# Performance work log

Hardware: AMD Instinct MI355X
Metric: run time of the kernel (lower is better)

Reference implementation:

```python
import jax, jax.numpy as jnp
import numpy as np

NUM_TRAIN = 256  # num_train_anchors
N, A, T = 8, 131072, 64


def _make_boxes(key, shape2):
    # shape2 = (..., 2) of (y, x); returns valid boxes (y1, x1, y2, x2) in [0, 1]
    k1, k2 = jax.random.split(key)
    c1 = jax.random.uniform(k1, shape2, dtype=jnp.float32)
    c2 = jax.random.uniform(k2, shape2, dtype=jnp.float32)
    lo = jnp.minimum(c1, c2)
    hi = jnp.maximum(c1, c2)
    return jnp.stack([lo[..., 0], lo[..., 1], hi[..., 0], hi[..., 1]], axis=-1)


def setup_inputs() -> dict:
    key = jax.random.key(0)
    ka, kt, kp, kn = jax.random.split(key, 4)
    return {
        "anchors": _make_boxes(ka, (N, A, 2)),
        "true_bboxes": _make_boxes(kt, (N, T, 2)),
        "rand_pos": jax.random.uniform(kp, (N, A), dtype=jnp.float32),
        "rand_neg": jax.random.uniform(kn, (N, A), dtype=jnp.float32),
    }


def _bbox_overlap(anchors, gt):
    # anchors [A,4], gt [T,4] -> IoU [A,T]
    ay1, ax1, ay2, ax2 = [anchors[:, i] for i in range(4)]
    gy1, gx1, gy2, gx2 = [gt[:, i] for i in range(4)]
    a_area = (ay2 - ay1) * (ax2 - ax1)                       # [A]
    g_area = (gy2 - gy1) * (gx2 - gx1)                       # [T]
    ih = jnp.clip(jnp.minimum(ay2[:, None], gy2[None, :]) - jnp.maximum(ay1[:, None], gy1[None, :]), 0.0)
    iw = jnp.clip(jnp.minimum(ax2[:, None], gx2[None, :]) - jnp.maximum(ax1[:, None], gx1[None, :]), 0.0)
    inter = ih * iw                                          # [A,T]
    union = a_area[:, None] + g_area[None, :] - inter
    return jnp.where(union > 0, inter / jnp.where(union > 0, union, 1.0), 0.0)


def _rank_of(scores):
    # rank[i] = position of element i in ascending sort of scores
    order = jnp.argsort(scores)
    return jnp.zeros(scores.shape[0], jnp.int32).at[order].set(jnp.arange(scores.shape[0], dtype=jnp.int32))


def _compute_bbox_deltas(anchors, gt):
    # standard (dy, dx, dh, dw) encoding with safe denominators
    ah = anchors[:, 2] - anchors[:, 0]
    aw = anchors[:, 3] - anchors[:, 1]
    acy = anchors[:, 0] + 0.5 * ah
    acx = anchors[:, 1] + 0.5 * aw
    gh = gt[:, 2] - gt[:, 0]
    gw = gt[:, 3] - gt[:, 1]
    gcy = gt[:, 0] + 0.5 * gh
    gcx = gt[:, 1] + 0.5 * gw
    ah_s = jnp.where(ah > 0, ah, 1.0)
    aw_s = jnp.where(aw > 0, aw, 1.0)
    gh_s = jnp.where(gh > 0, gh, 1.0)
    gw_s = jnp.where(gw > 0, gw, 1.0)
    return jnp.stack([(gcy - acy) / ah_s, (gcx - acx) / aw_s,
                      jnp.log(gh_s / ah_s), jnp.log(gw_s / aw_s)], axis=-1)


def _get_targets(anchors, gt, r_pos, r_neg):
    na = anchors.shape[0]
    # strip_out_of_bounds_anchors: zero out anchors falling outside [0,1]^2 (keeps static shape)
    inb = (anchors[:, 0] >= 0) & (anchors[:, 1] >= 0) & (anchors[:, 2] <= 1) & (anchors[:, 3] <= 1)
    anchors = jnp.where(inb[:, None], anchors, 0.0)

    overlaps = _bbox_overlap(anchors, gt)                    # [A,T]

    # --- class assignment ---
    iou_max_val = jnp.max(overlaps, axis=1)                  # [A]
    classes = jnp.full((na,), -1, jnp.int32)
    classes = jnp.where(iou_max_val < 0.3, 0, classes)
    iou_max_anchor = jnp.argmax(overlaps, axis=0)            # [T] best anchor per gt
    pos_anchor = jnp.zeros((na,), jnp.int32).at[iou_max_anchor].set(1)
    classes = jnp.where(pos_anchor > 0, 1, classes)
    classes = jnp.where(iou_max_val >= 0.7, 1, classes)

    # --- subsample positives to NUM_TRAIN//2 (uniform random subset) ---
    pos = classes > 0
    rank_p = _rank_of(jnp.where(pos, r_pos, jnp.inf))
    keep_pos = pos & (rank_p < NUM_TRAIN // 2)
    classes = jnp.where(pos & ~keep_pos, -1, classes)
    n_pos = jnp.sum(keep_pos.astype(jnp.int32))

    # --- subsample negatives to NUM_TRAIN - n_pos ---
    desired_neg = NUM_TRAIN - n_pos
    neg = classes == 0
    rank_n = _rank_of(jnp.where(neg, r_neg, jnp.inf))
    keep_neg = neg & (rank_n < desired_neg)
    classes = jnp.where(neg & ~keep_neg, -1, classes)

    # --- deltas for positive anchors ---
    best_gt = jnp.argmax(overlaps, axis=1)                   # [A]
    deltas = _compute_bbox_deltas(anchors, gt[best_gt])      # [A,4]
    deltas = jnp.where((classes > 0)[:, None], deltas, 0.0)
    return classes, deltas


def reference(anchors, true_bboxes, rand_pos, rand_neg):
    classes, deltas = jax.vmap(_get_targets)(anchors, true_bboxes, rand_pos, rand_neg)
    return classes, deltas
```

## Files before the change

kernel.cpp:

```cpp
#include <hip/hip_runtime.h>
#include <stdint.h>

#define N_B 8
#define A_N 131072
#define T_N 64
#define NUM_TRAIN 256
#define POS_CAP 65536
#define NEG_CAP 32768
#define NEG_TAU 0.05f
#define NB2 256
#define ITEM_CAP 1024
#define APT 4
#define GBLK (A_N / (256 * APT))
#define BLK_C (A_N / (256 * 4))

typedef unsigned long long u64;
typedef unsigned int u32;

__device__ __forceinline__ float iou_one(float ay1, float ax1, float ay2, float ax2,
                                         float a_area, float gy1, float gx1, float gy2,
                                         float gx2, float g_area) {
#pragma clang fp contract(off)
    float ih = fmaxf(fminf(ay2, gy2) - fmaxf(ay1, gy1), 0.0f);
    float iw = fmaxf(fminf(ax2, gx2) - fmaxf(ax1, gx1), 0.0f);
    float inter = ih * iw;
    float uni = (a_area + g_area) - inter;
    return uni > 0.0f ? inter / uni : 0.0f;
}

__global__ void __launch_bounds__(256, 4) k_main(const float4* __restrict__ anchors4,
                                                 const float4* __restrict__ gts4,
                                                 unsigned char* __restrict__ preclass,
                                                 u64* __restrict__ colpart) {
    __shared__ float4 gbox[T_N];
    __shared__ float gars[T_N];
    __shared__ u64 cmax[T_N];
    int n = blockIdx.y, tid = threadIdx.x, lane = tid & 63;
    int a0 = blockIdx.x * (256 * APT) + tid;
    if (tid < T_N) {
        float4 gb = gts4[n * T_N + tid];
        gbox[tid] = gb;
        {
#pragma clang fp contract(off)
            gars[tid] = (gb.z - gb.x) * (gb.w - gb.y);
        }
        cmax[tid] = 0xFFFFFFFFull;
    }
    __syncthreads();

    float ay1[APT], ax1[APT], ay2[APT], ax2[APT], aar[APT], vmax[APT];
#pragma unroll
    for (int k = 0; k < APT; k++) {
        float4 ab = anchors4[(size_t)n * A_N + a0 + k * 256];
        float y1 = ab.x, x1 = ab.y, y2 = ab.z, x2 = ab.w;
        bool inb = (y1 >= 0.f) && (x1 >= 0.f) && (y2 <= 1.f) && (x2 <= 1.f);
        if (!inb) { y1 = x1 = y2 = x2 = 0.f; }
        ay1[k] = y1; ax1[k] = x1; ay2[k] = y2; ax2[k] = x2;
        {
#pragma clang fp contract(off)
            aar[k] = (y2 - y1) * (x2 - x1);
        }
        vmax[k] = 0.f;
    }

#pragma unroll 2
    for (int jj = 0; jj < T_N; jj++) {
        int j = (lane + jj) & (T_N - 1);
        float4 gb = gbox[j];
        float gar = gars[j];
        u64 colc = 0;
#pragma unroll
        for (int k = 0; k < APT; k++) {
            float v = iou_one(ay1[k], ax1[k], ay2[k], ax2[k], aar[k],
                              gb.x, gb.y, gb.z, gb.w, gar);
            vmax[k] = fmaxf(vmax[k], v);
            u64 pcv = ((u64)__float_as_uint(v) << 32) | (u32)(~(u32)(a0 + k * 256));
            colc = pcv > colc ? pcv : colc;
        }
        atomicMax(&cmax[j], colc);
    }

#pragma unroll
    for (int k = 0; k < APT; k++) {
        float vm = vmax[k];
        int c0 = (vm < 0.3f) ? 0 : ((vm >= 0.7f) ? 1 : -1);
        preclass[(size_t)n * A_N + a0 + k * 256] = (unsigned char)(signed char)c0;
    }
    __syncthreads();
    if (tid < T_N) colpart[((size_t)n * T_N + tid) * GBLK + blockIdx.x] = cmax[tid];
}

__global__ void k_colred(const u64* __restrict__ colpart, int* __restrict__ wnr) {
    int w = blockIdx.x * 4 + (threadIdx.x >> 6);
    int lane = threadIdx.x & 63;
    const u64* p = colpart + (size_t)w * GBLK;
    u64 m = p[lane];
    u64 m2 = p[lane + 64];
    m = m2 > m ? m2 : m;
#pragma unroll
    for (int off = 32; off > 0; off >>= 1) {
        u64 o = (u64)__shfl_xor((unsigned long long)m, off, 64);
        m = o > m ? o : m;
    }
    if (lane == 0) wnr[w] = (int)(~(u32)(m & 0xFFFFFFFFull));
}

__global__ void __launch_bounds__(256) k_classify(const u32* __restrict__ preclass32,
                                                  const int* __restrict__ wnr,
                                                  const float4* __restrict__ rneg4,
                                                  u32* __restrict__ class32,
                                                  int* __restrict__ bcp, int* __restrict__ bcn) {
    __shared__ int wnrs[T_N];
    __shared__ int wp[4], wn[4];
    int n = blockIdx.y, bx = blockIdx.x, tid = threadIdx.x;
    if (tid < T_N) wnrs[tid] = wnr[n * T_N + tid];
    __syncthreads();

    size_t gi4 = ((size_t)n * A_N) / 4 + bx * 256 + tid;
    u32 pcw = preclass32[gi4];
    float4 rn = rneg4[gi4];
    int a0 = (bx * 256 + tid) * 4;

    u32 marked = 0;
#pragma unroll
    for (int t = 0; t < T_N; t++) {
        u32 d = (u32)(wnrs[t] - a0);
        if (d < 4u) marked |= 1u << d;
    }

    float rnv[4] = {rn.x, rn.y, rn.z, rn.w};
    int pcnt = 0, ncnt = 0;
    u32 cw = 0;
#pragma unroll
    for (int j = 0; j < 4; j++) {
        int c = (int)(signed char)((pcw >> (8 * j)) & 0xFF);
        if ((marked >> j) & 1) c = 1;
        cw |= ((u32)(unsigned char)(signed char)c) << (8 * j);
        pcnt += (c == 1);
        ncnt += (c == 0 && rnv[j] < NEG_TAU);
    }
    class32[gi4] = cw;

#pragma unroll
    for (int off = 32; off > 0; off >>= 1) {
        pcnt += __shfl_xor(pcnt, off, 64);
        ncnt += __shfl_xor(ncnt, off, 64);
    }
    if ((tid & 63) == 0) { wp[tid >> 6] = pcnt; wn[tid >> 6] = ncnt; }
    __syncthreads();
    if (tid == 0) {
        bcp[n * BLK_C + bx] = wp[0] + wp[1] + wp[2] + wp[3];
        bcn[n * BLK_C + bx] = wn[0] + wn[1] + wn[2] + wn[3];
    }
}

__global__ void __launch_bounds__(256) k_gather(const u32* __restrict__ class32,
                                                const float4* __restrict__ rpos4,
                                                const float4* __restrict__ rneg4,
                                                const int* __restrict__ bcp,
                                                const int* __restrict__ bcn,
                                                u64* __restrict__ pos_list,
                                                u64* __restrict__ neg_list) {
    __shared__ int sp[BLK_C], sn[BLK_C];
    __shared__ int lp, ln;
    int n = blockIdx.y, bx = blockIdx.x, tid = threadIdx.x;
    if (tid == 0) { lp = 0; ln = 0; }
    if (tid < BLK_C) { sp[tid] = bcp[n * BLK_C + tid]; sn[tid] = bcn[n * BLK_C + tid]; }
    __syncthreads();
    for (int d = 1; d < BLK_C; d <<= 1) {
        int vp = 0, vn = 0;
        if (tid < BLK_C && tid >= d) { vp = sp[tid - d]; vn = sn[tid - d]; }
        __syncthreads();
        if (tid < BLK_C) { sp[tid] += vp; sn[tid] += vn; }
        __syncthreads();
    }
    int bp = bx ? sp[bx - 1] : 0;
    int bn = bx ? sn[bx - 1] : 0;

    size_t gi4 = ((size_t)n * A_N) / 4 + bx * 256 + tid;
    u32 cw = class32[gi4];
    float4 rp = rpos4[gi4];
    float4 rn = rneg4[gi4];
    float rpv[4] = {rp.x, rp.y, rp.z, rp.w};
    float rnv[4] = {rn.x, rn.y, rn.z, rn.w};
    int a0 = (bx * 256 + tid) * 4;

#pragma unroll
    for (int j = 0; j < 4; j++) {
        int c = (int)(signed char)((cw >> (8 * j)) & 0xFF);
        int a = a0 + j;
        if (c == 1) {
            int slot = atomicAdd(&lp, 1);
            int i = bp + slot;
            if (i < POS_CAP)
                pos_list[n * POS_CAP + i] = ((u64)__float_as_uint(rpv[j]) << 32) | (u32)a;
        } else if (c == 0 && rnv[j] < NEG_TAU) {
            int slot = atomicAdd(&ln, 1);
            int i = bn + slot;
            if (i < NEG_CAP)
                neg_list[n * NEG_CAP + i] = ((u64)__float_as_uint(rnv[j]) << 32) | (u32)a;
        }
    }
}

__device__ u64 select_kth(const u64* list, int cnt, int k, float scale, u64 ovf,
                          int* hist, u64* items, int* misc, u64* result, int* wsum) {
    int tid = threadIdx.x, lane = tid & 63, wid = tid >> 6;
    if (k >= cnt) return ovf;

    hist[tid] = 0;
    if (tid == 0) { misc[0] = 0; *result = ovf; }
    __syncthreads();

    for (int i = tid; i < cnt; i += 256) {
        float v = __uint_as_float((u32)(list[i] >> 32));
        int b = (int)(v * scale); b = b < NB2 - 1 ? b : NB2 - 1;
        atomicAdd(&hist[b], 1);
    }
    __syncthreads();

    int h = hist[tid];
    int v = h;
#pragma unroll
    for (int d = 1; d < 64; d <<= 1) {
        int t = __shfl_up(v, d, 64);
        if (lane >= d) v += t;
    }
    if (lane == 63) wsum[wid] = v;
    __syncthreads();
    int base = 0;
    for (int w = 0; w < wid; w++) base += wsum[w];
    int incl = base + v, excl = incl - h;
    if (k >= excl && k < incl) { misc[1] = tid; misc[2] = excl; }
    __syncthreads();
    int b = misc[1], before = misc[2];

    for (int i = tid; i < cnt; i += 256) {
        u64 p = list[i];
        float vv = __uint_as_float((u32)(p >> 32));
        int bb = (int)(vv * scale); bb = bb < NB2 - 1 ? bb : NB2 - 1;
        if (bb == b) { int ix = atomicAdd(&misc[0], 1); if (ix < ITEM_CAP) items[ix] = p; }
    }
    __syncthreads();
    int m = misc[0]; m = m < ITEM_CAP ? m : ITEM_CAP;
    int target = k - before;
    for (int i = tid; i < m; i += 256) {
        u64 p = items[i];
        int r = 0;
        for (int j = 0; j < m; j++) r += (items[j] < p);
        if (r == target) *result = p;
    }
    __syncthreads();
    u64 res = *result;
    __syncthreads();
    return res;
}

__global__ void k_select(const u64* __restrict__ pos_list, const u64* __restrict__ neg_list,
                         const int* __restrict__ bcp, const int* __restrict__ bcn,
                         u64* __restrict__ cutoff) {
    __shared__ int hist[NB2];
    __shared__ u64 items[ITEM_CAP];
    __shared__ int misc[3];
    __shared__ u64 result;
    __shared__ int wsum[4];
    __shared__ int pw[4], nw[4];
    int n = blockIdx.x, tid = threadIdx.x;

    int pv = (tid < BLK_C) ? bcp[n * BLK_C + tid] : 0;
    int nv = (tid < BLK_C) ? bcn[n * BLK_C + tid] : 0;
#pragma unroll
    for (int off = 32; off > 0; off >>= 1) {
        pv += __shfl_xor(pv, off, 64);
        nv += __shfl_xor(nv, off, 64);
    }
    if ((tid & 63) == 0) { pw[tid >> 6] = pv; nw[tid >> 6] = nv; }
    __syncthreads();
    int P = pw[0] + pw[1] + pw[2] + pw[3];
    int C = nw[0] + nw[1] + nw[2] + nw[3];
    int Pc = P < POS_CAP ? P : POS_CAP;
    int Cc = C < NEG_CAP ? C : NEG_CAP;

    u64 cpos = select_kth(pos_list + n * POS_CAP, Pc, NUM_TRAIN / 2, (float)NB2,
                          0xFFFFFFFFFFFFFFFFull, hist, items, misc, &result, wsum);
    int n_pos = P < NUM_TRAIN / 2 ? P : NUM_TRAIN / 2;
    int k_neg = NUM_TRAIN - n_pos;
    u64 cneg = select_kth(neg_list + n * NEG_CAP, Cc, k_neg, (float)NB2 / NEG_TAU,
                          ((u64)__float_as_uint(NEG_TAU) << 32), hist, items, misc, &result, wsum);
    if (tid == 0) { cutoff[2 * n] = cpos; cutoff[2 * n + 1] = cneg; }
}

__global__ void __launch_bounds__(256) k_final(const float4* __restrict__ anchors4,
                                               const float4* __restrict__ gts4,
                                               const u32* __restrict__ class32,
                                               const float4* __restrict__ rpos4,
                                               const float4* __restrict__ rneg4,
                                               const u64* __restrict__ cutoff,
                                               float4* __restrict__ out_classes4,
                                               float4* __restrict__ out_deltas) {
    __shared__ float4 gbox[T_N];
    __shared__ float gars[T_N];
    int n = blockIdx.y, bx = blockIdx.x, tid = threadIdx.x;
    if (tid < T_N) {
        float4 gb = gts4[n * T_N + tid];
        gbox[tid] = gb;
        {
#pragma clang fp contract(off)
            gars[tid] = (gb.z - gb.x) * (gb.w - gb.y);
        }
    }
    __syncthreads();

    size_t gi4 = ((size_t)n * A_N) / 4 + bx * 256 + tid;
    u32 cw = class32[gi4];
    float4 rp = rpos4[gi4];
    float4 rn = rneg4[gi4];
    float rpv[4] = {rp.x, rp.y, rp.z, rp.w};
    float rnv[4] = {rn.x, rn.y, rn.z, rn.w};
    int a0 = (bx * 256 + tid) * 4;
    u64 cp = cutoff[2 * n], cn = cutoff[2 * n + 1];

    float fcv[4];
#pragma unroll
    for (int j = 0; j < 4; j++) {
        int c = (int)(signed char)((cw >> (8 * j)) & 0xFF);
        int a = a0 + j;
        int fc = -1;
        if (c == 1) {
            u64 p = ((u64)__float_as_uint(rpv[j]) << 32) | (u32)a;
            fc = (p < cp) ? 1 : -1;
        } else if (c == 0) {
            u64 p = ((u64)__float_as_uint(rnv[j]) << 32) | (u32)a;
            fc = (p < cn) ? 0 : -1;
        }
        fcv[j] = (float)fc;

        float4 d = make_float4(0.f, 0.f, 0.f, 0.f);
        if (fc == 1) {
            float4 ab = anchors4[(size_t)n * A_N + a];
            float ay1 = ab.x, ax1 = ab.y, ay2 = ab.z, ax2 = ab.w;
            bool inb = (ay1 >= 0.f) && (ax1 >= 0.f) && (ay2 <= 1.f) && (ax2 <= 1.f);
            if (!inb) { ay1 = ax1 = ay2 = ax2 = 0.f; }
            float a_area;
            {
#pragma clang fp contract(off)
                a_area = (ay2 - ay1) * (ax2 - ax1);
            }
            float vm = 0.f; int jb = 0;
            for (int t = 0; t < T_N; t++) {
                float4 gb = gbox[t];
                float v = iou_one(ay1, ax1, ay2, ax2, a_area, gb.x, gb.y, gb.z, gb.w, gars[t]);
                bool g = v > vm;
                vm = g ? v : vm;
                jb = g ? t : jb;
            }
            float4 gb = gbox[jb];
            float gy1 = gb.x, gx1 = gb.y, gy2 = gb.z, gx2 = gb.w;
            float ah = ay2 - ay1, aw = ax2 - ax1;
            float acy = ay1 + 0.5f * ah, acx = ax1 + 0.5f * aw;
            float gh = gy2 - gy1, gw = gx2 - gx1;
            float gcy = gy1 + 0.5f * gh, gcx = gx1 + 0.5f * gw;
            float ah_s = ah > 0.f ? ah : 1.f, aw_s = aw > 0.f ? aw : 1.f;
            float gh_s = gh > 0.f ? gh : 1.f, gw_s = gw > 0.f ? gw : 1.f;
            d.x = (gcy - acy) / ah_s;
            d.y = (gcx - acx) / aw_s;
            d.z = logf(gh_s / ah_s);
            d.w = logf(gw_s / aw_s);
        }
        out_deltas[(size_t)n * A_N + a] = d;
    }
    out_classes4[gi4] = make_float4(fcv[0], fcv[1], fcv[2], fcv[3]);
}

extern "C" void kernel_launch(void* const* d_in, const int* in_sizes, int n_in,
                              void* d_out, int out_size, void* d_ws, size_t ws_size,
                              hipStream_t stream) {
    const float* anchors = (const float*)d_in[0];
    const float* gts     = (const float*)d_in[1];
    const float* rpos    = (const float*)d_in[2];
    const float* rneg    = (const float*)d_in[3];

    char* p = (char*)d_ws;
    u64* cutoff   = (u64*)p;  p += 2 * N_B * sizeof(u64);
    u64* colpart  = (u64*)p;  p += (size_t)N_B * T_N * GBLK * sizeof(u64);
    u64* pos_list = (u64*)p;  p += (size_t)N_B * POS_CAP * sizeof(u64);
    u64* neg_list = (u64*)p;  p += (size_t)N_B * NEG_CAP * sizeof(u64);
    u32* preclass = (u32*)p;  p += (size_t)N_B * A_N;
    u32* class_f  = (u32*)p;  p += (size_t)N_B * A_N;
    int* bcp  = (int*)p;  p += N_B * BLK_C * sizeof(int);
    int* bcn  = (int*)p;  p += N_B * BLK_C * sizeof(int);
    int* wnr  = (int*)p;  p += N_B * T_N * sizeof(int);

    float* out_classes = (float*)d_out;
    float4* out_deltas = (float4*)(out_classes + (size_t)N_B * A_N);

    k_main<<<dim3(GBLK, N_B), 256, 0, stream>>>(
        (const float4*)anchors, (const float4*)gts, (unsigned char*)preclass, colpart);
    k_colred<<<N_B * T_N / 4, 256, 0, stream>>>(colpart, wnr);
    k_classify<<<dim3(BLK_C, N_B), 256, 0, stream>>>(
        preclass, wnr, (const float4*)rneg, class_f, bcp, bcn);
    k_gather<<<dim3(BLK_C, N_B), 256, 0, stream>>>(
        class_f, (const float4*)rpos, (const float4*)rneg, bcp, bcn, pos_list, neg_list);
    k_select<<<N_B, 256, 0, stream>>>(pos_list, neg_list, bcp, bcn, cutoff);
    k_final<<<dim3(BLK_C, N_B), 256, 0, stream>>>(
        (const float4*)anchors, (const float4*)gts, class_f,
        (const float4*)rpos, (const float4*)rneg, cutoff,
        (float4*)out_classes, out_deltas);
}
```

Measured before the change: 187.6 us.

## Fuse candidate gathering into IoU kernel and fold column reduction into select

The IoU kernel now writes positive and negative candidates straight into per-block segmented lists and records per-block counts. This removes the separate classify and gather passes and the colred kernel. The select kernel reduces the per-column argmax itself, adds the column-winner anchors as extra positives, and excludes them from the negative lists while it builds histograms. Six launches become three, and several full passes over classes and random values disappear. In exchange, select walks 128 segments per image and does a 64-way exclusion check for each negative candidate, and the inner IoU loop tracks a per-thread column argmax with a deeper unroll.

```diff
diff --git a/kernel.cpp b/kernel.cpp
--- a/kernel.cpp
+++ b/kernel.cpp
@@ -5,14 +5,11 @@
 #define A_N 131072
 #define T_N 64
 #define NUM_TRAIN 256
-#define POS_CAP 65536
-#define NEG_CAP 32768
 #define NEG_TAU 0.05f
-#define NB2 256
 #define ITEM_CAP 1024
 #define APT 4
-#define GBLK (A_N / (256 * APT))
-#define BLK_C (A_N / (256 * 4))
+#define GBLK 128
+#define SEG 1024
 
 typedef unsigned long long u64;
 typedef unsigned int u32;
@@ -30,13 +27,21 @@
 
 __global__ void __launch_bounds__(256, 4) k_main(const float4* __restrict__ anchors4,
                                                  const float4* __restrict__ gts4,
+                                                 const float* __restrict__ rpos,
+                                                 const float* __restrict__ rneg,
                                                  unsigned char* __restrict__ preclass,
-                                                 u64* __restrict__ colpart) {
+                                                 u64* __restrict__ colpart,
+                                                 u64* __restrict__ pos_list,
+                                                 u64* __restrict__ neg_list,
+                                                 int* __restrict__ bcp, int* __restrict__ bcn) {
     __shared__ float4 gbox[T_N];
     __shared__ float gars[T_N];
     __shared__ u64 cmax[T_N];
-    int n = blockIdx.y, tid = threadIdx.x, lane = tid & 63;
-    int a0 = blockIdx.x * (256 * APT) + tid;
+    __shared__ int lp, ln;
+    int n = blockIdx.y, bx = blockIdx.x, tid = threadIdx.x, lane = tid & 63;
+    int a0 = bx * SEG + tid;
+    size_t nA = (size_t)n * A_N;
+
     if (tid < T_N) {
         float4 gb = gts4[n * T_N + tid];
         gbox[tid] = gb;
@@ -44,14 +49,15 @@
 #pragma clang fp contract(off)
             gars[tid] = (gb.z - gb.x) * (gb.w - gb.y);
         }
-        cmax[tid] = 0xFFFFFFFFull;
-    }
+        cmax[tid] = 0;
+    }
+    if (tid == 0) { lp = 0; ln = 0; }
     __syncthreads();
 
     float ay1[APT], ax1[APT], ay2[APT], ax2[APT], aar[APT], vmax[APT];
 #pragma unroll
     for (int k = 0; k < APT; k++) {
-        float4 ab = anchors4[(size_t)n * A_N + a0 + k * 256];
+        float4 ab = anchors4[nA + a0 + k * 256];
         float y1 = ab.x, x1 = ab.y, y2 = ab.z, x2 = ab.w;
         bool inb = (y1 >= 0.f) && (x1 >= 0.f) && (y2 <= 1.f) && (x2 <= 1.f);
         if (!inb) { y1 = x1 = y2 = x2 = 0.f; }
@@ -63,164 +69,80 @@
         vmax[k] = 0.f;
     }
 
-#pragma unroll 2
+#pragma unroll 4
     for (int jj = 0; jj < T_N; jj++) {
         int j = (lane + jj) & (T_N - 1);
         float4 gb = gbox[j];
         float gar = gars[j];
-        u64 colc = 0;
-#pragma unroll
-        for (int k = 0; k < APT; k++) {
-            float v = iou_one(ay1[k], ax1[k], ay2[k], ax2[k], aar[k],
-                              gb.x, gb.y, gb.z, gb.w, gar);
+        float vb = iou_one(ay1[0], ax1[0], ay2[0], ax2[0], aar[0], gb.x, gb.y, gb.z, gb.w, gar);
+        vmax[0] = fmaxf(vmax[0], vb);
+        int kb = 0;
+#pragma unroll
+        for (int k = 1; k < APT; k++) {
+            float v = iou_one(ay1[k], ax1[k], ay2[k], ax2[k], aar[k], gb.x, gb.y, gb.z, gb.w, gar);
             vmax[k] = fmaxf(vmax[k], v);
-            u64 pcv = ((u64)__float_as_uint(v) << 32) | (u32)(~(u32)(a0 + k * 256));
-            colc = pcv > colc ? pcv : colc;
-        }
-        atomicMax(&cmax[j], colc);
-    }
-
+            if (v > vb) { vb = v; kb = k; }
+        }
+        u64 pk = ((u64)__float_as_uint(vb) << 32) | (u32)(~(u32)(a0 + (kb << 8)));
+        atomicMax(&cmax[j], pk);
+    }
+
+    size_t segbase = ((size_t)(n * GBLK + bx)) << 10;
 #pragma unroll
     for (int k = 0; k < APT; k++) {
+        int a = a0 + k * 256;
         float vm = vmax[k];
         int c0 = (vm < 0.3f) ? 0 : ((vm >= 0.7f) ? 1 : -1);
-        preclass[(size_t)n * A_N + a0 + k * 256] = (unsigned char)(signed char)c0;
-    }
-    __syncthreads();
-    if (tid < T_N) colpart[((size_t)n * T_N + tid) * GBLK + blockIdx.x] = cmax[tid];
-}
-
-__global__ void k_colred(const u64* __restrict__ colpart, int* __restrict__ wnr) {
-    int w = blockIdx.x * 4 + (threadIdx.x >> 6);
-    int lane = threadIdx.x & 63;
-    const u64* p = colpart + (size_t)w * GBLK;
-    u64 m = p[lane];
-    u64 m2 = p[lane + 64];
-    m = m2 > m ? m2 : m;
-#pragma unroll
-    for (int off = 32; off > 0; off >>= 1) {
-        u64 o = (u64)__shfl_xor((unsigned long long)m, off, 64);
-        m = o > m ? o : m;
-    }
-    if (lane == 0) wnr[w] = (int)(~(u32)(m & 0xFFFFFFFFull));
-}
-
-__global__ void __launch_bounds__(256) k_classify(const u32* __restrict__ preclass32,
-                                                  const int* __restrict__ wnr,
-                                                  const float4* __restrict__ rneg4,
-                                                  u32* __restrict__ class32,
-                                                  int* __restrict__ bcp, int* __restrict__ bcn) {
-    __shared__ int wnrs[T_N];
-    __shared__ int wp[4], wn[4];
-    int n = blockIdx.y, bx = blockIdx.x, tid = threadIdx.x;
-    if (tid < T_N) wnrs[tid] = wnr[n * T_N + tid];
-    __syncthreads();
-
-    size_t gi4 = ((size_t)n * A_N) / 4 + bx * 256 + tid;
-    u32 pcw = preclass32[gi4];
-    float4 rn = rneg4[gi4];
-    int a0 = (bx * 256 + tid) * 4;
-
-    u32 marked = 0;
-#pragma unroll
-    for (int t = 0; t < T_N; t++) {
-        u32 d = (u32)(wnrs[t] - a0);
-        if (d < 4u) marked |= 1u << d;
-    }
-
-    float rnv[4] = {rn.x, rn.y, rn.z, rn.w};
-    int pcnt = 0, ncnt = 0;
-    u32 cw = 0;
-#pragma unroll
-    for (int j = 0; j < 4; j++) {
-        int c = (int)(signed char)((pcw >> (8 * j)) & 0xFF);
-        if ((marked >> j) & 1) c = 1;
-        cw |= ((u32)(unsigned char)(signed char)c) << (8 * j);
-        pcnt += (c == 1);
-        ncnt += (c == 0 && rnv[j] < NEG_TAU);
-    }
-    class32[gi4] = cw;
-
-#pragma unroll
-    for (int off = 32; off > 0; off >>= 1) {
-        pcnt += __shfl_xor(pcnt, off, 64);
-        ncnt += __shfl_xor(ncnt, off, 64);
-    }
-    if ((tid & 63) == 0) { wp[tid >> 6] = pcnt; wn[tid >> 6] = ncnt; }
-    __syncthreads();
-    if (tid == 0) {
-        bcp[n * BLK_C + bx] = wp[0] + wp[1] + wp[2] + wp[3];
-        bcn[n * BLK_C + bx] = wn[0] + wn[1] + wn[2] + wn[3];
-    }
-}
-
-__global__ void __launch_bounds__(256) k_gather(const u32* __restrict__ class32,
-                                                const float4* __restrict__ rpos4,
-                                                const float4* __restrict__ rneg4,
-                                                const int* __restrict__ bcp,
-                                                const int* __restrict__ bcn,
-                                                u64* __restrict__ pos_list,
-                                                u64* __restrict__ neg_list) {
-    __shared__ int sp[BLK_C], sn[BLK_C];
-    __shared__ int lp, ln;
-    int n = blockIdx.y, bx = blockIdx.x, tid = threadIdx.x;
-    if (tid == 0) { lp = 0; ln = 0; }
-    if (tid < BLK_C) { sp[tid] = bcp[n * BLK_C + tid]; sn[tid] = bcn[n * BLK_C + tid]; }
-    __syncthreads();
-    for (int d = 1; d < BLK_C; d <<= 1) {
-        int vp = 0, vn = 0;
-        if (tid < BLK_C && tid >= d) { vp = sp[tid - d]; vn = sn[tid - d]; }
-        __syncthreads();
-        if (tid < BLK_C) { sp[tid] += vp; sn[tid] += vn; }
-        __syncthreads();
-    }
-    int bp = bx ? sp[bx - 1] : 0;
-    int bn = bx ? sn[bx - 1] : 0;
-
-    size_t gi4 = ((size_t)n * A_N) / 4 + bx * 256 + tid;
-    u32 cw = class32[gi4];
-    float4 rp = rpos4[gi4];
-    float4 rn = rneg4[gi4];
-    float rpv[4] = {rp.x, rp.y, rp.z, rp.w};
-    float rnv[4] = {rn.x, rn.y, rn.z, rn.w};
-    int a0 = (bx * 256 + tid) * 4;
-
-#pragma unroll
-    for (int j = 0; j < 4; j++) {
-        int c = (int)(signed char)((cw >> (8 * j)) & 0xFF);
-        int a = a0 + j;
-        if (c == 1) {
-            int slot = atomicAdd(&lp, 1);
-            int i = bp + slot;
-            if (i < POS_CAP)
-                pos_list[n * POS_CAP + i] = ((u64)__float_as_uint(rpv[j]) << 32) | (u32)a;
-        } else if (c == 0 && rnv[j] < NEG_TAU) {
-            int slot = atomicAdd(&ln, 1);
-            int i = bn + slot;
-            if (i < NEG_CAP)
-                neg_list[n * NEG_CAP + i] = ((u64)__float_as_uint(rnv[j]) << 32) | (u32)a;
-        }
-    }
-}
-
-__device__ u64 select_kth(const u64* list, int cnt, int k, float scale, u64 ovf,
-                          int* hist, u64* items, int* misc, u64* result, int* wsum) {
+        preclass[nA + a] = (unsigned char)(signed char)c0;
+        if (c0 == 1) {
+            int s = atomicAdd(&lp, 1);
+            pos_list[segbase + s] = ((u64)__float_as_uint(rpos[nA + a]) << 32) | (u32)a;
+        } else if (c0 == 0) {
+            float r = rneg[nA + a];
+            if (r < NEG_TAU) {
+                int s = atomicAdd(&ln, 1);
+                neg_list[segbase + s] = ((u64)__float_as_uint(r) << 32) | (u32)a;
+            }
+        }
+    }
+    __syncthreads();
+    if (tid < T_N) colpart[(size_t)((n << 6) + tid) * GBLK + bx] = cmax[tid];
+    if (tid == 0) { bcp[n * GBLK + bx] = lp; bcn[n * GBLK + bx] = ln; }
+}
+
+__device__ u64 select_seg(const u64* lists, const int* scnt, int nseg,
+                          const u64* extras, int ecnt, const int* excl,
+                          int k, float scale, u64 ovf_all,
+                          int* hist, u64* items, int* misc, int* wsum, u64* result) {
     int tid = threadIdx.x, lane = tid & 63, wid = tid >> 6;
-    if (k >= cnt) return ovf;
-
     hist[tid] = 0;
-    if (tid == 0) { misc[0] = 0; *result = ovf; }
-    __syncthreads();
-
-    for (int i = tid; i < cnt; i += 256) {
-        float v = __uint_as_float((u32)(list[i] >> 32));
-        int b = (int)(v * scale); b = b < NB2 - 1 ? b : NB2 - 1;
-        atomicAdd(&hist[b], 1);
-    }
-    __syncthreads();
-
-    int h = hist[tid];
-    int v = h;
+    if (tid == 0) { misc[0] = 0; *result = ovf_all; }
+    __syncthreads();
+
+    for (int blk = 0; blk < nseg; blk++) {
+        int c = scnt[blk];
+        const u64* b = lists + ((size_t)blk << 10);
+        for (int i = tid; i < c; i += 256) {
+            u64 p = b[i];
+            if (excl) {
+                int a = (int)(u32)p;
+                bool ex = false;
+                for (int t = 0; t < T_N; t++) ex |= (excl[t] == a);
+                if (ex) continue;
+            }
+            float v = __uint_as_float((u32)(p >> 32));
+            int bb = (int)(v * scale); bb = bb > 255 ? 255 : bb;
+            atomicAdd(&hist[bb], 1);
+        }
+    }
+    for (int i = tid; i < ecnt; i += 256) {
+        float v = __uint_as_float((u32)(extras[i] >> 32));
+        int bb = (int)(v * scale); bb = bb > 255 ? 255 : bb;
+        atomicAdd(&hist[bb], 1);
+    }
+    __syncthreads();
+
+    int h = hist[tid], v = h;
 #pragma unroll
     for (int d = 1; d < 64; d <<= 1) {
         int t = __shfl_up(v, d, 64);
@@ -230,16 +152,34 @@
     __syncthreads();
     int base = 0;
     for (int w = 0; w < wid; w++) base += wsum[w];
-    int incl = base + v, excl = incl - h;
-    if (k >= excl && k < incl) { misc[1] = tid; misc[2] = excl; }
-    __syncthreads();
+    int total = wsum[0] + wsum[1] + wsum[2] + wsum[3];
+    int incl = base + v, exc = incl - h;
+    if (k >= exc && k < incl) { misc[1] = tid; misc[2] = exc; }
+    __syncthreads();
+    if (k >= total) return ovf_all;
     int b = misc[1], before = misc[2];
 
-    for (int i = tid; i < cnt; i += 256) {
-        u64 p = list[i];
+    for (int blk = 0; blk < nseg; blk++) {
+        int c = scnt[blk];
+        const u64* bb2 = lists + ((size_t)blk << 10);
+        for (int i = tid; i < c; i += 256) {
+            u64 p = bb2[i];
+            if (excl) {
+                int a = (int)(u32)p;
+                bool ex = false;
+                for (int t = 0; t < T_N; t++) ex |= (excl[t] == a);
+                if (ex) continue;
+            }
+            float vv = __uint_as_float((u32)(p >> 32));
+            int bn = (int)(vv * scale); bn = bn > 255 ? 255 : bn;
+            if (bn == b) { int ix = atomicAdd(&misc[0], 1); if (ix < ITEM_CAP) items[ix] = p; }
+        }
+    }
+    for (int i = tid; i < ecnt; i += 256) {
+        u64 p = extras[i];
         float vv = __uint_as_float((u32)(p >> 32));
-        int bb = (int)(vv * scale); bb = bb < NB2 - 1 ? bb : NB2 - 1;
-        if (bb == b) { int ix = atomicAdd(&misc[0], 1); if (ix < ITEM_CAP) items[ix] = p; }
+        int bn = (int)(vv * scale); bn = bn > 255 ? 255 : bn;
+        if (bn == b) { int ix = atomicAdd(&misc[0], 1); if (ix < ITEM_CAP) items[ix] = p; }
     }
     __syncthreads();
     int m = misc[0]; m = m < ITEM_CAP ? m : ITEM_CAP;
@@ -256,43 +196,89 @@
     return res;
 }
 
-__global__ void k_select(const u64* __restrict__ pos_list, const u64* __restrict__ neg_list,
-                         const int* __restrict__ bcp, const int* __restrict__ bcn,
-                         u64* __restrict__ cutoff) {
-    __shared__ int hist[NB2];
+__global__ void __launch_bounds__(256) k_select(const u64* __restrict__ pos_list,
+                                                const u64* __restrict__ neg_list,
+                                                const int* __restrict__ bcp,
+                                                const int* __restrict__ bcn,
+                                                const u64* __restrict__ colpart,
+                                                const unsigned char* __restrict__ preclass,
+                                                const float* __restrict__ rpos,
+                                                int* __restrict__ wnr_g,
+                                                u64* __restrict__ cutoff) {
+    __shared__ int sbp[GBLK], sbn[GBLK];
+    __shared__ u64 cq[256];
+    __shared__ int wnrs[T_N];
+    __shared__ u64 extras[T_N];
+    __shared__ int hist[256];
     __shared__ u64 items[ITEM_CAP];
-    __shared__ int misc[3];
+    __shared__ int misc[4];
     __shared__ u64 result;
     __shared__ int wsum[4];
-    __shared__ int pw[4], nw[4];
-    int n = blockIdx.x, tid = threadIdx.x;
-
-    int pv = (tid < BLK_C) ? bcp[n * BLK_C + tid] : 0;
-    int nv = (tid < BLK_C) ? bcn[n * BLK_C + tid] : 0;
+    __shared__ int shr[9];
+    int n = blockIdx.x, tid = threadIdx.x, lane = tid & 63, wid = tid >> 6;
+
+    int pv = tid < GBLK ? bcp[n * GBLK + tid] : 0;
+    int nv = tid < GBLK ? bcn[n * GBLK + tid] : 0;
+    if (tid < GBLK) { sbp[tid] = pv; sbn[tid] = nv; }
 #pragma unroll
     for (int off = 32; off > 0; off >>= 1) {
         pv += __shfl_xor(pv, off, 64);
         nv += __shfl_xor(nv, off, 64);
     }
-    if ((tid & 63) == 0) { pw[tid >> 6] = pv; nw[tid >> 6] = nv; }
-    __syncthreads();
-    int P = pw[0] + pw[1] + pw[2] + pw[3];
-    int C = nw[0] + nw[1] + nw[2] + nw[3];
-    int Pc = P < POS_CAP ? P : POS_CAP;
-    int Cc = C < NEG_CAP ? C : NEG_CAP;
-
-    u64 cpos = select_kth(pos_list + n * POS_CAP, Pc, NUM_TRAIN / 2, (float)NB2,
-                          0xFFFFFFFFFFFFFFFFull, hist, items, misc, &result, wsum);
+    if (lane == 0) { shr[wid] = pv; shr[4 + wid] = nv; }
+
+    {
+        int t = tid >> 2, q = tid & 3;
+        const u64* cp = colpart + (size_t)((n << 6) + t) * GBLK + q * 32;
+        u64 m = 0;
+        for (int i = 0; i < 32; i++) { u64 x = cp[i]; m = x > m ? x : m; }
+        cq[tid] = m;
+    }
+    __syncthreads();
+    if (tid < T_N) {
+        u64 m = cq[tid * 4];
+        u64 x = cq[tid * 4 + 1]; m = x > m ? x : m;
+        x = cq[tid * 4 + 2]; m = x > m ? x : m;
+        x = cq[tid * 4 + 3]; m = x > m ? x : m;
+        int w = (int)(~(u32)(m & 0xFFFFFFFFull));
+        wnrs[tid] = w;
+        wnr_g[n * T_N + tid] = w;
+    }
+    __syncthreads();
+    if (tid < T_N) {
+        int w = wnrs[tid];
+        bool dup = false;
+        for (int t2 = 0; t2 < tid; t2++) dup |= (wnrs[t2] == w);
+        int pc = (int)(signed char)preclass[(size_t)n * A_N + w];
+        bool val = !dup && (pc != 1);
+        u64 mask = __ballot(val);
+        if (val) {
+            int ix = (int)__popcll(mask & ((1ull << lane) - 1));
+            extras[ix] = ((u64)__float_as_uint(rpos[(size_t)n * A_N + w]) << 32) | (u32)w;
+        }
+        if (tid == 0) shr[8] = (int)__popcll(mask);
+    }
+    __syncthreads();
+    int extra_cnt = shr[8];
+    int P = shr[0] + shr[1] + shr[2] + shr[3] + extra_cnt;
+
+    u64 cpos = select_seg(pos_list + (((size_t)n * GBLK) << 10), sbp, GBLK,
+                          extras, extra_cnt, nullptr,
+                          NUM_TRAIN / 2, 256.0f, ~0ull,
+                          hist, items, misc, wsum, &result);
     int n_pos = P < NUM_TRAIN / 2 ? P : NUM_TRAIN / 2;
     int k_neg = NUM_TRAIN - n_pos;
-    u64 cneg = select_kth(neg_list + n * NEG_CAP, Cc, k_neg, (float)NB2 / NEG_TAU,
-                          ((u64)__float_as_uint(NEG_TAU) << 32), hist, items, misc, &result, wsum);
+    u64 cneg = select_seg(neg_list + (((size_t)n * GBLK) << 10), sbn, GBLK,
+                          nullptr, 0, wnrs,
+                          k_neg, 256.0f / NEG_TAU, ((u64)__float_as_uint(NEG_TAU) << 32),
+                          hist, items, misc, wsum, &result);
     if (tid == 0) { cutoff[2 * n] = cpos; cutoff[2 * n + 1] = cneg; }
 }
 
 __global__ void __launch_bounds__(256) k_final(const float4* __restrict__ anchors4,
                                                const float4* __restrict__ gts4,
-                                               const u32* __restrict__ class32,
+                                               const u32* __restrict__ preclass32,
+                                               const int* __restrict__ wnr_g,
                                                const float4* __restrict__ rpos4,
                                                const float4* __restrict__ rneg4,
                                                const u64* __restrict__ cutoff,
@@ -300,6 +286,7 @@
                                                float4* __restrict__ out_deltas) {
     __shared__ float4 gbox[T_N];
     __shared__ float gars[T_N];
+    __shared__ int wnrs[T_N];
     int n = blockIdx.y, bx = blockIdx.x, tid = threadIdx.x;
     if (tid < T_N) {
         float4 gb = gts4[n * T_N + tid];
@@ -308,11 +295,12 @@
 #pragma clang fp contract(off)
             gars[tid] = (gb.z - gb.x) * (gb.w - gb.y);
         }
+        wnrs[tid] = wnr_g[n * T_N + tid];
     }
     __syncthreads();
 
     size_t gi4 = ((size_t)n * A_N) / 4 + bx * 256 + tid;
-    u32 cw = class32[gi4];
+    u32 pcw = preclass32[gi4];
     float4 rp = rpos4[gi4];
     float4 rn = rneg4[gi4];
     float rpv[4] = {rp.x, rp.y, rp.z, rp.w};
@@ -320,10 +308,18 @@
     int a0 = (bx * 256 + tid) * 4;
     u64 cp = cutoff[2 * n], cn = cutoff[2 * n + 1];
 
+    u32 marked = 0;
+#pragma unroll
+    for (int t = 0; t < T_N; t++) {
+        u32 d = (u32)(wnrs[t] - a0);
+        if (d < 4u) marked |= 1u << d;
+    }
+
     float fcv[4];
 #pragma unroll
     for (int j = 0; j < 4; j++) {
-        int c = (int)(signed char)((cw >> (8 * j)) & 0xFF);
+        int c = (int)(signed char)((pcw >> (8 * j)) & 0xFF);
+        if ((marked >> j) & 1) c = 1;
         int a = a0 + j;
         int fc = -1;
         if (c == 1) {
@@ -355,11 +351,10 @@
                 jb = g ? t : jb;
             }
             float4 gb = gbox[jb];
-            float gy1 = gb.x, gx1 = gb.y, gy2 = gb.z, gx2 = gb.w;
             float ah = ay2 - ay1, aw = ax2 - ax1;
             float acy = ay1 + 0.5f * ah, acx = ax1 + 0.5f * aw;
-            float gh = gy2 - gy1, gw = gx2 - gx1;
-            float gcy = gy1 + 0.5f * gh, gcx = gx1 + 0.5f * gw;
+            float gh = gb.z - gb.x, gw = gb.w - gb.y;
+            float gcy = gb.x + 0.5f * gh, gcx = gb.y + 0.5f * gw;
             float ah_s = ah > 0.f ? ah : 1.f, aw_s = aw > 0.f ? aw : 1.f;
             float gh_s = gh > 0.f ? gh : 1.f, gw_s = gw > 0.f ? gw : 1.f;
             d.x = (gcy - acy) / ah_s;
@@ -383,27 +378,23 @@
     char* p = (char*)d_ws;
     u64* cutoff   = (u64*)p;  p += 2 * N_B * sizeof(u64);
     u64* colpart  = (u64*)p;  p += (size_t)N_B * T_N * GBLK * sizeof(u64);
-    u64* pos_list = (u64*)p;  p += (size_t)N_B * POS_CAP * sizeof(u64);
-    u64* neg_list = (u64*)p;  p += (size_t)N_B * NEG_CAP * sizeof(u64);
-    u32* preclass = (u32*)p;  p += (size_t)N_B * A_N;
-    u32* class_f  = (u32*)p;  p += (size_t)N_B * A_N;
-    int* bcp  = (int*)p;  p += N_B * BLK_C * sizeof(int);
-    int* bcn  = (int*)p;  p += N_B * BLK_C * sizeof(int);
+    u64* pos_list = (u64*)p;  p += (size_t)N_B * GBLK * SEG * sizeof(u64);
+    u64* neg_list = (u64*)p;  p += (size_t)N_B * GBLK * SEG * sizeof(u64);
+    unsigned char* preclass = (unsigned char*)p; p += (size_t)N_B * A_N;
+    int* bcp  = (int*)p;  p += N_B * GBLK * sizeof(int);
+    int* bcn  = (int*)p;  p += N_B * GBLK * sizeof(int);
     int* wnr  = (int*)p;  p += N_B * T_N * sizeof(int);
 
     float* out_classes = (float*)d_out;
     float4* out_deltas = (float4*)(out_classes + (size_t)N_B * A_N);
 
     k_main<<<dim3(GBLK, N_B), 256, 0, stream>>>(
-        (const float4*)anchors, (const float4*)gts, (unsigned char*)preclass, colpart);
-    k_colred<<<N_B * T_N / 4, 256, 0, stream>>>(colpart, wnr);
-    k_classify<<<dim3(BLK_C, N_B), 256, 0, stream>>>(
-        preclass, wnr, (const float4*)rneg, class_f, bcp, bcn);
-    k_gather<<<dim3(BLK_C, N_B), 256, 0, stream>>>(
-        class_f, (const float4*)rpos, (const float4*)rneg, bcp, bcn, pos_list, neg_list);
-    k_select<<<N_B, 256, 0, stream>>>(pos_list, neg_list, bcp, bcn, cutoff);
-    k_final<<<dim3(BLK_C, N_B), 256, 0, stream>>>(
-        (const float4*)anchors, (const float4*)gts, class_f,
+        (const float4*)anchors, (const float4*)gts, rpos, rneg,
+        preclass, colpart, pos_list, neg_list, bcp, bcn);
+    k_select<<<N_B, 256, 0, stream>>>(pos_list, neg_list, bcp, bcn, colpart,
+                                      preclass, rpos, wnr, cutoff);
+    k_final<<<dim3(GBLK, N_B), 256, 0, stream>>>(
+        (const float4*)anchors, (const float4*)gts, (const u32*)preclass, wnr,
         (const float4*)rpos, (const float4*)rneg, cutoff,
         (float4*)out_classes, out_deltas);
 }
```

Measured after the change: 423.3 us. 2.26x slower.
